# Optimization experiments

Measured on AMD Instinct MI355X. Metric: run time of the kernel, lower is better.

The kernel has to match this reference:

```python
import jax, jax.numpy as jnp
import numpy as np

# ---- config (mirrors DecodeSSDPredictions init kwargs) ----
IMG_H, IMG_W = 512, 512
NMS_MAX = 100          # nms_max_output_size: greedy NMS iterations
CONF_T = 0.5           # confidence_threshold
IOU_T = 0.35           # iou_threshold
NUM_PRED = 10          # num_predictions (final top-k)
B, N_BOXES, N_CLASSES = 32, 24564, 81  # class 0 = background


def setup_inputs() -> dict:
    key = jax.random.key(0)
    k1, k2, k3, k4 = jax.random.split(key, 4)
    # class confidences: softmax of sharp logits so a fraction pass conf>=0.5
    cls = jax.nn.softmax(jax.random.normal(k1, (B, N_BOXES, N_CLASSES), jnp.float32) * 3.0, axis=-1)
    # predicted offsets (cx, cy, log w, log h deltas)
    offsets = jax.random.normal(k2, (B, N_BOXES, 4), jnp.float32) * 0.5
    # anchor priors: centers in (0,1), sizes in (0.05, 0.3)
    cxcy = jax.random.uniform(k3, (B, N_BOXES, 2), jnp.float32, 0.05, 0.95)
    wh = jax.random.uniform(k4, (B, N_BOXES, 2), jnp.float32, 0.05, 0.30)
    variances = jnp.broadcast_to(jnp.array([0.1, 0.1, 0.2, 0.2], jnp.float32), (B, N_BOXES, 4))
    y_pred = jnp.concatenate([cls, offsets, cxcy, wh, variances], axis=-1)  # [B, N, C+12]
    return {"y_pred": y_pred}


def _iou(boxes, box):
    # boxes: [N,4] corners (xmin,ymin,xmax,ymax); box: [4]
    iw = jnp.clip(jnp.minimum(boxes[:, 2], box[2]) - jnp.maximum(boxes[:, 0], box[0]), 0.0)
    ih = jnp.clip(jnp.minimum(boxes[:, 3], box[3]) - jnp.maximum(boxes[:, 1], box[1]), 0.0)
    inter = iw * ih
    area_b = (boxes[:, 2] - boxes[:, 0]) * (boxes[:, 3] - boxes[:, 1])
    area_q = (box[2] - box[0]) * (box[3] - box[1])
    return inter / (area_b + area_q - inter + 1e-12)


def _per_item(rows6):
    # rows6: [N, 6] = (class_id, score, xmin, ymin, xmax, ymax)
    neg_inf = jnp.float32(-jnp.inf)
    valid = (rows6[:, 0] != 0) & (rows6[:, 1] >= CONF_T)  # drop background + low conf
    scores0 = jnp.where(valid, rows6[:, 1], neg_inf)
    boxes = rows6[:, 2:6]

    def body(i, carry):
        alive, kept_idx, kept_sc = carry
        idx = jnp.argmax(alive)
        best = alive[idx]
        ok = best > neg_inf
        kept_idx = kept_idx.at[i].set(jnp.where(ok, idx.astype(jnp.int32), -1))
        kept_sc = kept_sc.at[i].set(jnp.where(ok, best, neg_inf))
        # suppress overlapping boxes (incl. the selected one, iou=1 > thr)
        sup = _iou(boxes, boxes[idx]) > IOU_T
        alive = jnp.where(ok & sup, neg_inf, alive)
        return alive, kept_idx, kept_sc

    carry0 = (scores0,
              jnp.full((NMS_MAX,), -1, jnp.int32),
              jnp.full((NMS_MAX,), neg_inf, jnp.float32))
    _, kept_idx, kept_sc = jax.lax.fori_loop(0, NMS_MAX, body, carry0)

    kept_rows = rows6[jnp.clip(kept_idx, 0)]            # [NMS_MAX, 6]
    top_sc, top_i = jax.lax.top_k(kept_sc, NUM_PRED)    # final top-k by score
    out = kept_rows[top_i]
    return jnp.where(jnp.isfinite(top_sc)[:, None], out, 0.0)


def reference(y_pred):
    cls = y_pred[..., :-12]
    # SSD box decode
    cx = y_pred[..., -12] * y_pred[..., -4] * y_pred[..., -6] + y_pred[..., -8]
    cy = y_pred[..., -11] * y_pred[..., -3] * y_pred[..., -5] + y_pred[..., -7]
    w = jnp.exp(y_pred[..., -10] * y_pred[..., -2]) * y_pred[..., -6]
    h = jnp.exp(y_pred[..., -9] * y_pred[..., -1]) * y_pred[..., -5]
    xmin = (cx - 0.5 * w) * IMG_W
    ymin = (cy - 0.5 * h) * IMG_H
    xmax = (cx + 0.5 * w) * IMG_W
    ymax = (cy + 0.5 * h) * IMG_H
    class_id = jnp.argmax(cls, axis=-1).astype(y_pred.dtype)
    score = jnp.max(cls, axis=-1)
    rows = jnp.stack([class_id, score, xmin, ymin, xmax, ymax], axis=-1)  # [B, N, 6]
    return jax.vmap(_per_item)(rows)  # [B, NUM_PRED, 6]
```

## Files before the change

kernel.cpp:

```cpp
#include <hip/hip_runtime.h>
#include <math.h>

#define B 32
#define NBOX 24564
#define NCLS 81
#define ROWLEN 93
#define CONF_T 0.5f
#define IOU_T 0.35f
#define NUM_PRED 10
#define IMG_W 512.0f
#define IMG_H 512.0f

#define BPB 64
#define K1_THREADS 256
#define NBLK ((NBOX + BPB - 1) / BPB)

#define K2T 1024
#define NPER ((NBOX + K2T - 1) / K2T)

__global__ __launch_bounds__(K1_THREADS) void decode_kernel(
    const float* __restrict__ y, float4* __restrict__ boxes,
    float* __restrict__ scores, float* __restrict__ clsid)
{
    __shared__ float4 lds4[(BPB * ROWLEN) / 4];
    float* lds = (float*)lds4;
    int bid  = blockIdx.x;
    int b    = bid / NBLK;
    int blk  = bid % NBLK;
    int box0 = blk * BPB;
    int nb   = NBOX - box0; if (nb > BPB) nb = BPB;
    int n4   = (nb * ROWLEN) / 4;
    const float4* src = (const float4*)(y + ((size_t)b * NBOX + box0) * ROWLEN);
    for (int k = threadIdx.x; k < n4; k += K1_THREADS)
        lds4[k] = src[k];
    __syncthreads();

    int q  = threadIdx.x & 3;
    int bl = threadIdx.x >> 2;
    if (bl >= nb) return;
    const float* row = &lds[bl * ROWLEN];

    float best = -INFINITY; int bci = 0x7fffffff;
    for (int c = q; c < NCLS; c += 4) {
        float v = row[c];
        if (v > best) { best = v; bci = c; }
    }
    #pragma unroll
    for (int m = 1; m <= 2; m <<= 1) {
        float ov = __shfl_xor(best, m, 64);
        int   oi = __shfl_xor(bci,  m, 64);
        if (ov > best || (ov == best && oi < bci)) { best = ov; bci = oi; }
    }

    if (q == 0) {
        const float* t = row + NCLS;
        float cx = t[0] * t[8]  * t[6] + t[4];
        float cy = t[1] * t[9]  * t[7] + t[5];
        float w  = expf(t[2] * t[10]) * t[6];
        float h  = expf(t[3] * t[11]) * t[7];
        float4 bx;
        bx.x = (cx - 0.5f * w) * IMG_W;
        bx.y = (cy - 0.5f * h) * IMG_H;
        bx.z = (cx + 0.5f * w) * IMG_W;
        bx.w = (cy + 0.5f * h) * IMG_H;
        size_t g = (size_t)b * NBOX + box0 + bl;
        boxes[g] = bx;
        clsid[g] = (float)bci;
        bool valid = (bci != 0) && (best >= CONF_T);
        scores[g] = valid ? best : -INFINITY;
    }
}

__global__ __launch_bounds__(K2T) void nms_kernel(
    const float4* __restrict__ boxes, const float* __restrict__ scores,
    const float* __restrict__ clsid, float* __restrict__ out)
{
    __shared__ float pv[16];
    __shared__ int   pi[16];
    __shared__ float bvS;
    __shared__ int   biS;
    int b = blockIdx.x, tid = threadIdx.x;
    int lane = tid & 63, wid = tid >> 6;
    const float4* bxp = boxes  + (size_t)b * NBOX;
    const float*  scp = scores + (size_t)b * NBOX;

    float sc[NPER];
    #pragma unroll
    for (int j = 0; j < NPER; j++) {
        int g = j * K2T + tid;
        sc[j] = (g < NBOX) ? scp[g] : -INFINITY;
    }

    float4 qb = make_float4(0.f, 0.f, 0.f, 0.f);
    float  aq = 0.f;
    bool   have_pick = false;

    for (int r = 0; r < NUM_PRED; r++) {
        float v = -INFINITY; int idx = -1;
        #pragma unroll
        for (int j = 0; j < NPER; j++) {
            float s = sc[j];
            if (s > -INFINITY) {
                if (have_pick) {
                    int g = j * K2T + tid;
                    float4 p = bxp[g];
                    float iw = fmaxf(fminf(p.z, qb.z) - fmaxf(p.x, qb.x), 0.0f);
                    float ih = fmaxf(fminf(p.w, qb.w) - fmaxf(p.y, qb.y), 0.0f);
                    float inter = iw * ih;
                    float ab = (p.z - p.x) * (p.w - p.y);
                    float iou = inter / (ab + aq - inter + 1e-12f);
                    if (iou > IOU_T) { s = -INFINITY; sc[j] = s; }
                }
                if (s > v) { v = s; idx = j * K2T + tid; }
            }
        }
        #pragma unroll
        for (int m = 1; m < 64; m <<= 1) {
            float ov = __shfl_xor(v, m, 64);
            int   oi = __shfl_xor(idx, m, 64);
            if (ov > v) { v = ov; idx = oi; }
        }
        if (lane == 0) { pv[wid] = v; pi[wid] = idx; }
        __syncthreads();
        if (wid == 0) {
            float v2 = (lane < 16) ? pv[lane] : -INFINITY;
            int   i2 = (lane < 16) ? pi[lane] : -1;
            #pragma unroll
            for (int m = 1; m < 16; m <<= 1) {
                float ov = __shfl_xor(v2, m, 64);
                int   oi = __shfl_xor(i2, m, 64);
                if (ov > v2) { v2 = ov; i2 = oi; }
            }
            if (lane == 0) { bvS = v2; biS = i2; }
        }
        __syncthreads();
        float bv = bvS; int bi = biS;

        if (!(bv > -INFINITY)) {
            if (tid == 0) {
                for (int rr = r; rr < NUM_PRED; rr++) {
                    float* o = out + ((size_t)b * NUM_PRED + rr) * 6;
                    for (int k = 0; k < 6; k++) o[k] = 0.0f;
                }
            }
            return;
        }

        qb = bxp[bi];
        aq = (qb.z - qb.x) * (qb.w - qb.y);
        have_pick = true;
        if (tid == 0) {
            float* o = out + ((size_t)b * NUM_PRED + r) * 6;
            o[0] = clsid[(size_t)b * NBOX + bi];
            o[1] = bv;
            o[2] = qb.x; o[3] = qb.y; o[4] = qb.z; o[5] = qb.w;
        }
    }
}

extern "C" void kernel_launch(void* const* d_in, const int* in_sizes, int n_in,
                              void* d_out, int out_size, void* d_ws, size_t ws_size,
                              hipStream_t stream) {
    const float* y = (const float*)d_in[0];
    float* out = (float*)d_out;
    char* ws = (char*)d_ws;
    float4* boxes  = (float4*)ws;
    float*  scores = (float*)(ws + (size_t)B * NBOX * sizeof(float4));
    float*  clsidp = scores + (size_t)B * NBOX;

    decode_kernel<<<B * NBLK, K1_THREADS, 0, stream>>>(y, boxes, scores, clsidp);
    nms_kernel<<<B, K2T, 0, stream>>>(boxes, scores, clsidp, out);
}
```

Before: 465.1 us.

## Compact valid candidates with wave atomics and cache NMS boxes in registers

The decode kernel now writes only boxes that pass the confidence and background filter. It packs them into a per-image compacted list, using a wave ballot plus one atomicAdd per wave, and a memset clears the counters first. The NMS kernel loads the compacted scores and boxes into registers once, so each suppression round stops re-reading boxes from global memory and works on fewer candidates. Candidates beyond the register capacity fall back to LDS scores and global box reads. The compacted order is nondeterministic, so ties in score could be broken differently than before.

After: 873.3 us. 87.8% more time.

```diff
diff --git a/kernel.cpp b/kernel.cpp
--- a/kernel.cpp
+++ b/kernel.cpp
@@ -16,11 +16,15 @@
 #define NBLK ((NBOX + BPB - 1) / BPB)
 
 #define K2T 1024
-#define NPER ((NBOX + K2T - 1) / K2T)
+#define NPER_R 12
+#define CAP_SLOTS (K2T * NPER_R)
+#define NPER_ALL ((NBOX + K2T - 1) / K2T)
+#define NPER_OV (NPER_ALL - NPER_R)
 
 __global__ __launch_bounds__(K1_THREADS) void decode_kernel(
-    const float* __restrict__ y, float4* __restrict__ boxes,
-    float* __restrict__ scores, float* __restrict__ clsid)
+    const float* __restrict__ y, float4* __restrict__ cboxes,
+    float* __restrict__ cscores, float* __restrict__ cclsid,
+    int* __restrict__ cnt)
 {
     __shared__ float4 lds4[(BPB * ROWLEN) / 4];
     float* lds = (float*)lds4;
@@ -51,44 +55,69 @@
         int   oi = __shfl_xor(bci,  m, 64);
         if (ov > best || (ov == best && oi < bci)) { best = ov; bci = oi; }
     }
-
-    if (q == 0) {
-        const float* t = row + NCLS;
-        float cx = t[0] * t[8]  * t[6] + t[4];
-        float cy = t[1] * t[9]  * t[7] + t[5];
-        float w  = expf(t[2] * t[10]) * t[6];
-        float h  = expf(t[3] * t[11]) * t[7];
-        float4 bx;
-        bx.x = (cx - 0.5f * w) * IMG_W;
-        bx.y = (cy - 0.5f * h) * IMG_H;
-        bx.z = (cx + 0.5f * w) * IMG_W;
-        bx.w = (cy + 0.5f * h) * IMG_H;
-        size_t g = (size_t)b * NBOX + box0 + bl;
-        boxes[g] = bx;
-        clsid[g] = (float)bci;
-        bool valid = (bci != 0) && (best >= CONF_T);
-        scores[g] = valid ? best : -INFINITY;
+    bool valid = (bci != 0) && (best >= CONF_T);
+    bool pred  = (q == 0) && valid;
+
+    unsigned long long m = __ballot(pred);
+    if (m != 0ull) {
+        int lane   = threadIdx.x & 63;
+        int leader = __ffsll((unsigned long long)m) - 1;
+        int base   = 0;
+        if (lane == leader) base = atomicAdd(&cnt[b], __popcll(m));
+        base = __shfl(base, leader, 64);
+        if (pred) {
+            int rank = __popcll(m & ((1ull << lane) - 1ull));
+            int pos  = base + rank;
+            const float* t = row + NCLS;
+            float cx = t[0] * t[8]  * t[6] + t[4];
+            float cy = t[1] * t[9]  * t[7] + t[5];
+            float w  = expf(t[2] * t[10]) * t[6];
+            float h  = expf(t[3] * t[11]) * t[7];
+            float4 bx;
+            bx.x = (cx - 0.5f * w) * IMG_W;
+            bx.y = (cy - 0.5f * h) * IMG_H;
+            bx.z = (cx + 0.5f * w) * IMG_W;
+            bx.w = (cy + 0.5f * h) * IMG_H;
+            size_t g = (size_t)b * NBOX + pos;
+            cboxes[g]  = bx;
+            cscores[g] = best;
+            cclsid[g]  = (float)bci;
+        }
     }
 }
 
 __global__ __launch_bounds__(K2T) void nms_kernel(
-    const float4* __restrict__ boxes, const float* __restrict__ scores,
-    const float* __restrict__ clsid, float* __restrict__ out)
+    const float4* __restrict__ cboxes, const float* __restrict__ cscores,
+    const float* __restrict__ cclsid, const int* __restrict__ cnt,
+    float* __restrict__ out)
 {
+    __shared__ float ovsc[NPER_OV * K2T];
     __shared__ float pv[16];
     __shared__ int   pi[16];
     __shared__ float bvS;
     __shared__ int   biS;
     int b = blockIdx.x, tid = threadIdx.x;
     int lane = tid & 63, wid = tid >> 6;
-    const float4* bxp = boxes  + (size_t)b * NBOX;
-    const float*  scp = scores + (size_t)b * NBOX;
-
-    float sc[NPER];
+    int n = cnt[b];
+    const float4* bxp = cboxes  + (size_t)b * NBOX;
+    const float*  scp = cscores + (size_t)b * NBOX;
+
+    float  sreg[NPER_R];
+    float4 breg[NPER_R];
     #pragma unroll
-    for (int j = 0; j < NPER; j++) {
+    for (int j = 0; j < NPER_R; j++) {
         int g = j * K2T + tid;
-        sc[j] = (g < NBOX) ? scp[g] : -INFINITY;
+        bool in = (g < n);
+        sreg[j] = in ? scp[g] : -INFINITY;
+        breg[j] = in ? bxp[g] : make_float4(0.f, 0.f, 0.f, 0.f);
+    }
+    bool ovf = (n > CAP_SLOTS);
+    if (ovf) {
+        #pragma unroll
+        for (int j = 0; j < NPER_OV; j++) {
+            int g = (NPER_R + j) * K2T + tid;
+            ovsc[j * K2T + tid] = (g < n) ? scp[g] : -INFINITY;
+        }
     }
 
     float4 qb = make_float4(0.f, 0.f, 0.f, 0.f);
@@ -98,20 +127,38 @@
     for (int r = 0; r < NUM_PRED; r++) {
         float v = -INFINITY; int idx = -1;
         #pragma unroll
-        for (int j = 0; j < NPER; j++) {
-            float s = sc[j];
+        for (int j = 0; j < NPER_R; j++) {
+            float s = sreg[j];
             if (s > -INFINITY) {
                 if (have_pick) {
-                    int g = j * K2T + tid;
-                    float4 p = bxp[g];
+                    float4 p = breg[j];
                     float iw = fmaxf(fminf(p.z, qb.z) - fmaxf(p.x, qb.x), 0.0f);
                     float ih = fmaxf(fminf(p.w, qb.w) - fmaxf(p.y, qb.y), 0.0f);
                     float inter = iw * ih;
                     float ab = (p.z - p.x) * (p.w - p.y);
                     float iou = inter / (ab + aq - inter + 1e-12f);
-                    if (iou > IOU_T) { s = -INFINITY; sc[j] = s; }
+                    if (iou > IOU_T) { s = -INFINITY; sreg[j] = s; }
                 }
                 if (s > v) { v = s; idx = j * K2T + tid; }
+            }
+        }
+        if (ovf) {
+            #pragma unroll
+            for (int j = 0; j < NPER_OV; j++) {
+                float s = ovsc[j * K2T + tid];
+                if (s > -INFINITY) {
+                    int g = (NPER_R + j) * K2T + tid;
+                    if (have_pick) {
+                        float4 p = bxp[g];
+                        float iw = fmaxf(fminf(p.z, qb.z) - fmaxf(p.x, qb.x), 0.0f);
+                        float ih = fmaxf(fminf(p.w, qb.w) - fmaxf(p.y, qb.y), 0.0f);
+                        float inter = iw * ih;
+                        float ab = (p.z - p.x) * (p.w - p.y);
+                        float iou = inter / (ab + aq - inter + 1e-12f);
+                        if (iou > IOU_T) { s = -INFINITY; ovsc[j * K2T + tid] = s; }
+                    }
+                    if (s > v) { v = s; idx = g; }
+                }
             }
         }
         #pragma unroll
@@ -151,7 +198,7 @@
         have_pick = true;
         if (tid == 0) {
             float* o = out + ((size_t)b * NUM_PRED + r) * 6;
-            o[0] = clsid[(size_t)b * NBOX + bi];
+            o[0] = cclsid[(size_t)b * NBOX + bi];
             o[1] = bv;
             o[2] = qb.x; o[3] = qb.y; o[4] = qb.z; o[5] = qb.w;
         }
@@ -164,10 +211,12 @@
     const float* y = (const float*)d_in[0];
     float* out = (float*)d_out;
     char* ws = (char*)d_ws;
-    float4* boxes  = (float4*)ws;
-    float*  scores = (float*)(ws + (size_t)B * NBOX * sizeof(float4));
-    float*  clsidp = scores + (size_t)B * NBOX;
-
-    decode_kernel<<<B * NBLK, K1_THREADS, 0, stream>>>(y, boxes, scores, clsidp);
-    nms_kernel<<<B, K2T, 0, stream>>>(boxes, scores, clsidp, out);
+    float4* cboxes  = (float4*)ws;
+    float*  cscores = (float*)(ws + (size_t)B * NBOX * sizeof(float4));
+    float*  cclsid  = cscores + (size_t)B * NBOX;
+    int*    cnt     = (int*)(cclsid + (size_t)B * NBOX);
+
+    hipMemsetAsync(cnt, 0, B * sizeof(int), stream);
+    decode_kernel<<<B * NBLK, K1_THREADS, 0, stream>>>(y, cboxes, cscores, cclsid, cnt);
+    nms_kernel<<<B, K2T, 0, stream>>>(cboxes, cscores, cclsid, cnt, out);
 }
```
